# Performance work log

Measured on AMD Instinct MI355X. Metric: run time of the kernel, lower is better.

## Reference

```python
import jax, jax.numpy as jnp
import numpy as np

N = 262144      # nodes per graph
NC = 65536      # common nodes
D = 256         # feature_dim


def setup_inputs() -> dict:
    key = jax.random.key(0)
    ks = jax.random.split(key, 12)
    h_prop = jax.random.normal(ks[0], (N, D), dtype=jnp.float32)
    h_context = jax.random.normal(ks[1], (N, D), dtype=jnp.float32)
    h_orig = jax.random.normal(ks[2], (NC, D), dtype=jnp.float32)
    # unique indices (torch scatter-assign semantics are only well-defined without dups)
    idx_prop = jnp.sort(jax.random.permutation(ks[3], N)[:NC]).astype(jnp.int64)
    idx_ctx = jnp.sort(jax.random.permutation(ks[4], N)[:NC]).astype(jnp.int64)
    # parameters (xavier-ish scale)
    s = 1.0 / np.sqrt(D)
    w_orig = jax.random.normal(ks[5], (D, D), dtype=jnp.float32) * s
    w_prop = jax.random.normal(ks[6], (D, D), dtype=jnp.float32) * s
    w_ctx = jax.random.normal(ks[7], (D, D), dtype=jnp.float32) * s
    W_fuse = jax.random.normal(ks[8], (D, 3 * D), dtype=jnp.float32) * (1.0 / np.sqrt(3 * D))  # torch Linear weight (out,in)
    b_fuse = jnp.zeros((D,), dtype=jnp.float32)
    bias = jax.random.uniform(ks[9], (D,), dtype=jnp.float32, minval=-s, maxval=s)
    return {
        "h_prop": h_prop, "h_context": h_context,
        "h_original_common_nodes": h_orig,
        "w_orig": w_orig, "w_prop": w_prop, "w_ctx": w_ctx,
        "W_fuse": W_fuse, "b_fuse": b_fuse, "bias": bias,
        "common_node_indices_in_prop": idx_prop,
        "common_node_indices_in_context": idx_ctx,
    }


def reference(h_prop, h_context, h_original_common_nodes,
              w_orig, w_prop, w_ctx, W_fuse, b_fuse, bias,
              common_node_indices_in_prop, common_node_indices_in_context):
    # gather common rows + three small GEMMs  [NC, D]
    t_orig = h_original_common_nodes @ w_orig
    t_prop = h_prop[common_node_indices_in_prop] @ w_prop
    t_ctx = h_context[common_node_indices_in_context] @ w_ctx
    # concat-linear-tanh-bias  [NC, D]
    fused = jnp.concatenate([t_orig, t_prop, t_ctx], axis=1) @ W_fuse.T + b_fuse
    fused = jnp.tanh(fused) + bias
    # scatter update into clones of the full tables
    h_prop_updated = h_prop.at[common_node_indices_in_prop].set(fused)
    h_context_updated = h_context.at[common_node_indices_in_context].set(fused)
    return (h_prop_updated, h_context_updated)
```

## Files before the change

### kernel.cpp

```cpp
#include <hip/hip_runtime.h>
#include <hip/hip_bf16.h>
#include <math.h>

#define NN 262144
#define NCC 65536

typedef __bf16 bf16x8 __attribute__((ext_vector_type(8)));
typedef __bf16 bf16x4 __attribute__((ext_vector_type(4)));
typedef float f32x4 __attribute__((ext_vector_type(4)));

__global__ __launch_bounds__(256) void k_setup(const float* __restrict__ w_orig,
                                               const float* __restrict__ w_prop,
                                               const float* __restrict__ w_ctx,
                                               const float* __restrict__ W_fuse,
                                               __bf16* __restrict__ Mt,
                                               unsigned char* __restrict__ flags) {
    __shared__ float Wl[64 * 65];
    __shared__ float wl[64 * 65];
    int b = blockIdx.x;
    int t = threadIdx.x;
    if (b >= 48) {
        ((uint4*)flags)[(b - 48) * 256 + t] = make_uint4(0u, 0u, 0u, 0u);
        return;
    }
    int seg = b >> 4, rem = b & 15;
    int ot = rem >> 2, mt = rem & 3;
    const float* wseg = seg == 0 ? w_orig : (seg == 1 ? w_prop : w_ctx);
    int to = (t & 15) * 4, tm = (t >> 4) * 4;
    float acc[4][4] = {};
    for (int kc = 0; kc < 4; ++kc) {
        __syncthreads();
        for (int i = 0; i < 16; ++i) {
            int f = i * 256 + t;
            int row = f >> 6, col = f & 63;
            Wl[row * 65 + col] = W_fuse[(size_t)(ot * 64 + row) * 768 + seg * 256 + kc * 64 + col];
            wl[row * 65 + col] = wseg[(size_t)(mt * 64 + row) * 256 + kc * 64 + col];
        }
        __syncthreads();
        for (int k = 0; k < 64; ++k) {
            float wo[4], wm2[4];
#pragma unroll
            for (int i = 0; i < 4; ++i) wo[i] = Wl[(to + i) * 65 + k];
#pragma unroll
            for (int j = 0; j < 4; ++j) wm2[j] = wl[(tm + j) * 65 + k];
#pragma unroll
            for (int i = 0; i < 4; ++i)
#pragma unroll
                for (int j = 0; j < 4; ++j) acc[i][j] += wo[i] * wm2[j];
        }
    }
    for (int i = 0; i < 4; ++i)
        for (int j = 0; j < 4; ++j) {
            int o = ot * 64 + to + i;
            int g = seg * 256 + mt * 64 + tm + j;
            Mt[(size_t)o * 768 + g] = (__bf16)acc[i][j];
        }
}

__global__ void k_setflags(const int* __restrict__ idxp, const int* __restrict__ idxc,
                           unsigned char* fp, unsigned char* fc) {
    int j = blockIdx.x * blockDim.x + threadIdx.x;
    if (j < NCC) { fp[idxp[j]] = 1; fc[idxc[j]] = 1; }
}

#define MFMA __builtin_amdgcn_mfma_f32_16x16x32_bf16

__global__ __launch_bounds__(256, 4) void k_main(const float* __restrict__ hp,
                                                 const float* __restrict__ hc,
                                                 const float* __restrict__ horig,
                                                 const __bf16* __restrict__ Mt,
                                                 const float* __restrict__ bfuse,
                                                 const float* __restrict__ bias,
                                                 const int* __restrict__ idxp,
                                                 const int* __restrict__ idxc,
                                                 const unsigned char* __restrict__ fp,
                                                 const unsigned char* __restrict__ fc,
                                                 float* __restrict__ out0,
                                                 float* __restrict__ out1) {
    __shared__ __align__(16) char smem[16384];
    int g = blockIdx.x;
    int role = (g >> 3) & 1;
    int bid = ((g >> 4) << 3) | (g & 7);
    int t = threadIdx.x;

    if (role == 0) {
        int tbl = bid >= 1024;
        int r0 = (tbl ? bid - 1024 : bid) << 8;
        const unsigned char* F = tbl ? fc : fp;
        const float* S = tbl ? hc : hp;
        float* D = tbl ? out1 : out0;
#pragma unroll
        for (int gg = 0; gg < 8; ++gg) {
            unsigned char fl[8];
            f32x4 v[8];
#pragma unroll
            for (int i = 0; i < 8; ++i) {
                int item = (gg * 8 + i) * 256 + t;
                fl[i] = F[r0 + (item >> 6)];
            }
#pragma unroll
            for (int i = 0; i < 8; ++i) {
                int item = (gg * 8 + i) * 256 + t;
                int r = r0 + (item >> 6), slot = item & 63;
                v[i] = *(const f32x4*)(S + (size_t)(fl[i] ? r0 : r) * 256 + slot * 4);
            }
#pragma unroll
            for (int i = 0; i < 8; ++i) {
                int item = (gg * 8 + i) * 256 + t;
                int r = r0 + (item >> 6), slot = item & 63;
                if (!fl[i]) __builtin_nontemporal_store(v[i], (f32x4*)(D + (size_t)r * 256 + slot * 4));
            }
        }
        return;
    }

    int jbase = bid * 32;
    int lane = t & 63, wid = t >> 6;
    int l15 = lane & 15, lq = lane >> 4;

    const __bf16* bp[4];
#pragma unroll
    for (int ni = 0; ni < 4; ++ni)
        bp[ni] = Mt + (size_t)(wid * 64 + ni * 16 + l15) * 768 + lq * 8;

    f32x4 acc[2][4] = {};

#pragma unroll
    for (int seg = 0; seg < 3; ++seg) {
        __syncthreads();
#pragma unroll
        for (int b2 = 0; b2 < 2; ++b2) {
            f32x4 v[4];
#pragma unroll
            for (int i = 0; i < 4; ++i) {
                int r = wid * 8 + b2 * 4 + i;
                int j = jbase + r;
                const float* src = seg == 0 ? horig + (size_t)j * 256
                                 : seg == 1 ? hp + (size_t)idxp[j] * 256
                                            : hc + (size_t)idxc[j] * 256;
                v[i] = *(const f32x4*)(src + lane * 4);
            }
#pragma unroll
            for (int i = 0; i < 4; ++i) {
                int r = wid * 8 + b2 * 4 + i;
                bf16x4 w;
                w[0] = (__bf16)v[i][0]; w[1] = (__bf16)v[i][1];
                w[2] = (__bf16)v[i][2]; w[3] = (__bf16)v[i][3];
                int off = lq * 4096 + r * 128 + ((((l15) >> 1) ^ (r & 7)) << 4) + (l15 & 1) * 8;
                *(bf16x4*)(smem + off) = w;
            }
        }
        __syncthreads();
#pragma unroll
        for (int c = 0; c < 4; ++c) {
            int cg = seg * 4 + c;
            bf16x8 bfr[4][2];
#pragma unroll
            for (int ni = 0; ni < 4; ++ni)
#pragma unroll
                for (int ks = 0; ks < 2; ++ks)
                    bfr[ni][ks] = *(const bf16x8*)(bp[ni] + cg * 64 + ks * 32);
            bf16x8 af[2][2];
#pragma unroll
            for (int mi = 0; mi < 2; ++mi)
#pragma unroll
                for (int ks = 0; ks < 2; ++ks) {
                    int row = mi * 16 + l15;
                    int sl = ks * 4 + lq;
                    af[mi][ks] = *(const bf16x8*)(smem + c * 4096 + row * 128 + ((sl ^ (row & 7)) << 4));
                }
#pragma unroll
            for (int ks = 0; ks < 2; ++ks)
#pragma unroll
                for (int mi = 0; mi < 2; ++mi)
#pragma unroll
                    for (int ni = 0; ni < 4; ++ni)
                        acc[mi][ni] = MFMA(af[mi][ks], bfr[ni][ks], acc[mi][ni], 0, 0, 0);
        }
    }

    float bfv[4], biv[4];
#pragma unroll
    for (int ni = 0; ni < 4; ++ni) {
        int o = wid * 64 + ni * 16 + l15;
        bfv[ni] = bfuse[o];
        biv[ni] = bias[o];
    }
    __syncthreads();
    float* scr = (float*)(smem + wid * 4096);
#pragma unroll
    for (int mi = 0; mi < 2; ++mi) {
#pragma unroll
        for (int ni = 0; ni < 4; ++ni)
#pragma unroll
            for (int rr = 0; rr < 4; ++rr) {
                float v = tanhf(acc[mi][ni][rr] + bfv[ni]) + biv[ni];
                scr[(lq * 4 + rr) * 64 + ni * 16 + l15] = v;
            }
#pragma unroll
        for (int rnd = 0; rnd < 4; ++rnd) {
            int rr2 = rnd * 4 + lq;
            int j = jbase + mi * 16 + rr2;
            int gp = idxp[j], gc = idxc[j];
            f32x4 v = *(const f32x4*)&scr[rr2 * 64 + l15 * 4];
            *(f32x4*)(out0 + (size_t)gp * 256 + wid * 64 + l15 * 4) = v;
            *(f32x4*)(out1 + (size_t)gc * 256 + wid * 64 + l15 * 4) = v;
        }
    }
}

extern "C" void kernel_launch(void* const* d_in, const int* in_sizes, int n_in,
                              void* d_out, int out_size, void* d_ws, size_t ws_size,
                              hipStream_t stream) {
    const float* hp     = (const float*)d_in[0];
    const float* hc     = (const float*)d_in[1];
    const float* horig  = (const float*)d_in[2];
    const float* w_orig = (const float*)d_in[3];
    const float* w_prop = (const float*)d_in[4];
    const float* w_ctx  = (const float*)d_in[5];
    const float* W_fuse = (const float*)d_in[6];
    const float* bfuse  = (const float*)d_in[7];
    const float* bias   = (const float*)d_in[8];
    const int* idxp     = (const int*)d_in[9];
    const int* idxc     = (const int*)d_in[10];
    float* out0 = (float*)d_out;
    float* out1 = out0 + (size_t)NN * 256;

    char* ws = (char*)d_ws;
    __bf16* Mt = (__bf16*)ws;
    unsigned char* fp = (unsigned char*)(ws + 393216);
    unsigned char* fc = fp + NN;

    k_setup<<<176, 256, 0, stream>>>(w_orig, w_prop, w_ctx, W_fuse, Mt, fp);
    k_setflags<<<NCC / 256, 256, 0, stream>>>(idxp, idxc, fp, fc);
    k_main<<<4096, 256, 0, stream>>>(hp, hc, horig, Mt, bfuse, bias,
                                     idxp, idxc, fp, fc, out0, out1);
}
```

Baseline: 335.3 us.

## Use 512-thread blocks with 64-row GEMM tiles and register-prefetched gathers

Doubles the block size to 512 threads. GEMM blocks now handle 64 common rows with a 2x4 wave layout over a full-width 256-column bf16 tile in 32KB LDS, and the next segment's gathered rows are prefetched into registers while the current segment is computed. Copy blocks become interleaved even/odd blocks that each copy 512 rows using plain stores instead of nontemporal stores, and flagged rows read row 0 instead of r0. This aims to overlap gather latency with MFMA work and to halve the number of B-fragment loads per output row. It costs higher register pressure and fewer, larger blocks, and it drops the nontemporal hint on the bulk copy.

```diff
diff --git a/kernel.cpp b/kernel.cpp
--- a/kernel.cpp
+++ b/kernel.cpp
@@ -65,7 +65,7 @@
 
 #define MFMA __builtin_amdgcn_mfma_f32_16x16x32_bf16
 
-__global__ __launch_bounds__(256, 4) void k_main(const float* __restrict__ hp,
+__global__ __launch_bounds__(512, 4) void k_main(const float* __restrict__ hp,
                                                  const float* __restrict__ hc,
                                                  const float* __restrict__ horig,
                                                  const __bf16* __restrict__ Mt,
@@ -77,77 +77,79 @@
                                                  const unsigned char* __restrict__ fc,
                                                  float* __restrict__ out0,
                                                  float* __restrict__ out1) {
-    __shared__ __align__(16) char smem[16384];
-    int g = blockIdx.x;
-    int role = (g >> 3) & 1;
-    int bid = ((g >> 4) << 3) | (g & 7);
+    __shared__ __align__(16) char smem[32768];
+    int bid = blockIdx.x >> 1;
     int t = threadIdx.x;
 
-    if (role == 0) {
-        int tbl = bid >= 1024;
-        int r0 = (tbl ? bid - 1024 : bid) << 8;
+    if (!(blockIdx.x & 1)) {
+        int tbl = bid >= 512;
         const unsigned char* F = tbl ? fc : fp;
         const float* S = tbl ? hc : hp;
         float* D = tbl ? out1 : out0;
-#pragma unroll
-        for (int gg = 0; gg < 8; ++gg) {
+        int r0 = (tbl ? bid - 512 : bid) * 512;
+#pragma unroll
+        for (int g = 0; g < 8; ++g) {
             unsigned char fl[8];
             f32x4 v[8];
 #pragma unroll
             for (int i = 0; i < 8; ++i) {
-                int item = (gg * 8 + i) * 256 + t;
-                fl[i] = F[r0 + (item >> 6)];
-            }
-#pragma unroll
-            for (int i = 0; i < 8; ++i) {
-                int item = (gg * 8 + i) * 256 + t;
-                int r = r0 + (item >> 6), slot = item & 63;
-                v[i] = *(const f32x4*)(S + (size_t)(fl[i] ? r0 : r) * 256 + slot * 4);
-            }
-#pragma unroll
-            for (int i = 0; i < 8; ++i) {
-                int item = (gg * 8 + i) * 256 + t;
-                int r = r0 + (item >> 6), slot = item & 63;
-                if (!fl[i]) __builtin_nontemporal_store(v[i], (f32x4*)(D + (size_t)r * 256 + slot * 4));
+                int gl = (g * 8 + i) * 512 + t;
+                fl[i] = F[r0 + (gl >> 6)];
+            }
+#pragma unroll
+            for (int i = 0; i < 8; ++i) {
+                int gl = (g * 8 + i) * 512 + t;
+                int r = r0 + (gl >> 6), slot = gl & 63;
+                v[i] = *(const f32x4*)(S + (size_t)(fl[i] ? 0 : r) * 256 + slot * 4);
+            }
+#pragma unroll
+            for (int i = 0; i < 8; ++i) {
+                int gl = (g * 8 + i) * 512 + t;
+                int r = r0 + (gl >> 6), slot = gl & 63;
+                if (!fl[i]) *(f32x4*)(D + (size_t)r * 256 + slot * 4) = v[i];
             }
         }
         return;
     }
 
-    int jbase = bid * 32;
+    int jbase = bid * 64;
     int lane = t & 63, wid = t >> 6;
+    int wm = wid >> 2, wn = wid & 3;
     int l15 = lane & 15, lq = lane >> 4;
 
     const __bf16* bp[4];
 #pragma unroll
     for (int ni = 0; ni < 4; ++ni)
-        bp[ni] = Mt + (size_t)(wid * 64 + ni * 16 + l15) * 768 + lq * 8;
+        bp[ni] = Mt + (size_t)(wn * 64 + ni * 16 + l15) * 768 + lq * 8;
 
     f32x4 acc[2][4] = {};
 
+    f32x4 v[8];
+#pragma unroll
+    for (int i = 0; i < 8; ++i)
+        v[i] = *(const f32x4*)(horig + (size_t)(jbase + wid * 8 + i) * 256 + lane * 4);
+
 #pragma unroll
     for (int seg = 0; seg < 3; ++seg) {
-        __syncthreads();
-#pragma unroll
-        for (int b2 = 0; b2 < 2; ++b2) {
-            f32x4 v[4];
-#pragma unroll
-            for (int i = 0; i < 4; ++i) {
-                int r = wid * 8 + b2 * 4 + i;
-                int j = jbase + r;
-                const float* src = seg == 0 ? horig + (size_t)j * 256
-                                 : seg == 1 ? hp + (size_t)idxp[j] * 256
-                                            : hc + (size_t)idxc[j] * 256;
+        bf16x4 w[8];
+#pragma unroll
+        for (int i = 0; i < 8; ++i) {
+            w[i][0] = (__bf16)v[i][0]; w[i][1] = (__bf16)v[i][1];
+            w[i][2] = (__bf16)v[i][2]; w[i][3] = (__bf16)v[i][3];
+        }
+        __syncthreads();
+#pragma unroll
+        for (int i = 0; i < 8; ++i) {
+            int r = wid * 8 + i;
+            *(bf16x4*)(smem + r * 512 + ((lane * 8) ^ ((r & 7) << 4))) = w[i];
+        }
+        if (seg < 2) {
+#pragma unroll
+            for (int i = 0; i < 8; ++i) {
+                int j = jbase + wid * 8 + i;
+                const float* src = (seg == 0) ? hp + (size_t)idxp[j] * 256
+                                              : hc + (size_t)idxc[j] * 256;
                 v[i] = *(const f32x4*)(src + lane * 4);
-            }
-#pragma unroll
-            for (int i = 0; i < 4; ++i) {
-                int r = wid * 8 + b2 * 4 + i;
-                bf16x4 w;
-                w[0] = (__bf16)v[i][0]; w[1] = (__bf16)v[i][1];
-                w[2] = (__bf16)v[i][2]; w[3] = (__bf16)v[i][3];
-                int off = lq * 4096 + r * 128 + ((((l15) >> 1) ^ (r & 7)) << 4) + (l15 & 1) * 8;
-                *(bf16x4*)(smem + off) = w;
             }
         }
         __syncthreads();
@@ -165,9 +167,9 @@
             for (int mi = 0; mi < 2; ++mi)
 #pragma unroll
                 for (int ks = 0; ks < 2; ++ks) {
-                    int row = mi * 16 + l15;
-                    int sl = ks * 4 + lq;
-                    af[mi][ks] = *(const bf16x8*)(smem + c * 4096 + row * 128 + ((sl ^ (row & 7)) << 4));
+                    int row = wm * 32 + mi * 16 + l15;
+                    int boff = (c * 128 + ks * 64 + lq * 16) ^ ((row & 7) << 4);
+                    af[mi][ks] = *(const bf16x8*)(smem + row * 512 + boff);
                 }
 #pragma unroll
             for (int ks = 0; ks < 2; ++ks)
@@ -182,7 +184,7 @@
     float bfv[4], biv[4];
 #pragma unroll
     for (int ni = 0; ni < 4; ++ni) {
-        int o = wid * 64 + ni * 16 + l15;
+        int o = wn * 64 + ni * 16 + l15;
         bfv[ni] = bfuse[o];
         biv[ni] = bias[o];
     }
@@ -194,17 +196,17 @@
         for (int ni = 0; ni < 4; ++ni)
 #pragma unroll
             for (int rr = 0; rr < 4; ++rr) {
-                float v = tanhf(acc[mi][ni][rr] + bfv[ni]) + biv[ni];
-                scr[(lq * 4 + rr) * 64 + ni * 16 + l15] = v;
+                float v2 = tanhf(acc[mi][ni][rr] + bfv[ni]) + biv[ni];
+                scr[(lq * 4 + rr) * 64 + ni * 16 + l15] = v2;
             }
 #pragma unroll
         for (int rnd = 0; rnd < 4; ++rnd) {
             int rr2 = rnd * 4 + lq;
-            int j = jbase + mi * 16 + rr2;
+            int j = jbase + wm * 32 + mi * 16 + rr2;
             int gp = idxp[j], gc = idxc[j];
-            f32x4 v = *(const f32x4*)&scr[rr2 * 64 + l15 * 4];
-            *(f32x4*)(out0 + (size_t)gp * 256 + wid * 64 + l15 * 4) = v;
-            *(f32x4*)(out1 + (size_t)gc * 256 + wid * 64 + l15 * 4) = v;
+            f32x4 vv = *(const f32x4*)&scr[rr2 * 64 + l15 * 4];
+            *(f32x4*)(out0 + (size_t)gp * 256 + wn * 64 + l15 * 4) = vv;
+            *(f32x4*)(out1 + (size_t)gc * 256 + wn * 64 + l15 * 4) = vv;
         }
     }
 }
@@ -233,6 +235,6 @@
 
     k_setup<<<176, 256, 0, stream>>>(w_orig, w_prop, w_ctx, W_fuse, Mt, fp);
     k_setflags<<<NCC / 256, 256, 0, stream>>>(idxp, idxc, fp, fc);
-    k_main<<<4096, 256, 0, stream>>>(hp, hc, horig, Mt, bfuse, bias,
+    k_main<<<2048, 512, 0, stream>>>(hp, hc, horig, Mt, bfuse, bias,
                                      idxp, idxc, fp, fc, out0, out1);
 }
```

Result: slower. 352.0 us (+5.0%).
